# Kernel optimization log

Hardware: AMD Instinct MI355X
Metric: run time of the kernel (lower is better)

Reference implementation:

```python
import jax, jax.numpy as jnp
import numpy as np

STD = 0.02

def setup_inputs() -> dict:
    key = jax.random.key(0)
    k1, k2, k3 = jax.random.split(key, 3)
    b, n_t, n, n_h = 2, 2048, 256, 8
    r_prime = jax.random.normal(k1, (b, n_t, n), dtype=jnp.float32)
    Q = STD * jax.random.normal(k2, (n_h, n, n), dtype=jnp.float32)
    E = STD * jax.random.normal(k3, (n_h, n, n), dtype=jnp.float32)
    return {"r_prime": r_prime, "Q": Q, "E": E}

def reference(r_prime, Q, E):
    # Omega[b,h,t,u] = sum_ij r'[b,t,i] Q[h,i,j] r'[b,u,j]
    Omega = jnp.einsum('bti,hij,buj->bhtu', r_prime, Q, r_prime)
    n_t = r_prime.shape[1]
    mask = jnp.tril(jnp.ones((n_t, n_t), dtype=r_prime.dtype))  # causal
    Omega = Omega * mask  # broadcast over (b, h)
    # r[b,t,i] = sum_{h,u,j} Omega[b,h,t,u] E[h,i,j] r'[b,u,j]
    r = jnp.einsum('bhtu,hij,buj->bti', Omega, E, r_prime)
    return r
```

## Files before the change

### kernel.cpp

```cpp
#include <hip/hip_runtime.h>
#include <hip/hip_bf16.h>

typedef __bf16 bf16x8 __attribute__((ext_vector_type(8)));
typedef float f32x4 __attribute__((ext_vector_type(4)));
typedef float f32x16 __attribute__((ext_vector_type(16)));

#define NB 2
#define NT 2048
#define ND 256
#define NH 8

__device__ inline __bf16 to_bf16(float f) {
  union { __hip_bfloat16 h; __bf16 b; } u;
  u.h = __float2bfloat16(f);
  return u.b;
}
__device__ inline float bf2f(__bf16 b) {
  union { __bf16 b; unsigned short s; } u; u.b = b;
  union { unsigned int i; float f; } v; v.i = ((unsigned int)u.s) << 16;
  return v.f;
}

typedef __attribute__((address_space(1))) const void g1void;
typedef __attribute__((address_space(3))) void l3void;

__device__ inline void gl_lds16(const void* g, void* l) {
  __builtin_amdgcn_global_load_lds((g1void*)g, (l3void*)l, 16, 0, 0);
}

__device__ inline void stage_tile64_t256(const __bf16* gsrc, __bf16* lds, int tid) {
  const char* wub = (const char*)lds + (tid & ~63) * 16;
#pragma unroll
  for (int p = 0; p < 8; ++p) {
    int lin = p * 256 + tid;
    int row = lin >> 5, c = lin & 31;
    const __bf16* g = gsrc + row * 256 + ((c ^ (row & 31)) << 3);
    gl_lds16((const void*)g, (void*)(wub + p * 4096));
  }
}

__device__ inline void stage_R64(const __bf16* gsrc, __bf16* lds, int w, int lane) {
#pragma unroll
  for (int p = 0; p < 4; ++p) {
    int lin = (p * 8 + w) * 64 + lane;
    int row = lin >> 5, c = lin & 31;
    const __bf16* g = gsrc + row * 256 + ((c ^ (row & 31)) << 3);
    gl_lds16((const void*)g, (void*)((char*)lds + (size_t)(p * 8 + w) * 1024));
  }
}
__device__ inline void stage_V64(const __bf16* gsrc, __bf16* lds, int w, int lane) {
#pragma unroll
  for (int p = 0; p < 4; ++p) {
    int lin = (p * 8 + w) * 64 + lane;
    int row = lin >> 3, c = lin & 7;
    const __bf16* g = gsrc + (size_t)row * NT + ((c ^ (row & 7)) << 3);
    gl_lds16((const void*)g, (void*)((char*)lds + (size_t)(p * 8 + w) * 1024));
  }
}

__global__ __launch_bounds__(256) void prep_kernel(
    const float* __restrict__ r, const float* __restrict__ Q,
    const float* __restrict__ E, __bf16* __restrict__ Rb,
    __bf16* __restrict__ Qt, __bf16* __restrict__ Eb) {
  __shared__ float T[32][33];
  int bx = blockIdx.x;
  if (bx < 512) {
    int h = bx >> 6, i0 = ((bx >> 3) & 7) * 32, j0 = (bx & 7) * 32;
    int rr = threadIdx.x >> 3, c4 = (threadIdx.x & 7) * 4;
    f32x4 v = *(const f32x4*)(Q + h * 65536 + (i0 + rr) * 256 + j0 + c4);
#pragma unroll
    for (int j = 0; j < 4; ++j) T[rr][c4 + j] = v[j];
    __syncthreads();
    __bf16* dst = Qt + h * 65536 + (j0 + rr) * 256 + i0 + c4;
#pragma unroll
    for (int j = 0; j < 4; ++j) dst[j] = to_bf16(T[c4 + j][rr]);
  } else {
    int idx = (bx - 512) * 256 + threadIdx.x;
    const int nR = NB * NT * ND;
    const int nQ = NH * ND * ND;
    const int stride = 1024 * 256;
    for (; idx < nR + nQ; idx += stride) {
      if (idx < nR) Rb[idx] = to_bf16(r[idx]);
      else Eb[idx - nR] = to_bf16(E[idx - nR]);
    }
  }
}

__global__ __launch_bounds__(256, 4) void gemm_stage1(
    const __bf16* __restrict__ Rb, const __bf16* __restrict__ Qt,
    const __bf16* __restrict__ Eb, __bf16* __restrict__ Am,
    __bf16* __restrict__ Vt) {
  __shared__ __bf16 Bs[64 * 256];
  int z = blockIdx.z, x = blockIdx.x;
  const __bf16 *A, *B;
  __bf16* C;
  int m0, n0, cstride;
  if (z < 16) {
    int bb = z >> 3, h = z & 7;
    A = Rb + (size_t)bb * NT * ND;
    B = Qt + (size_t)h * ND * ND;
    C = Am + (size_t)z * NT * ND;
    m0 = (x & 31) * 64; n0 = (x >> 5) * 64; cstride = ND;
  } else {
    int zz = z - 16;
    int bb = zz >> 3, h = zz & 7;
    A = Eb + (size_t)h * ND * ND;
    B = Rb + (size_t)bb * NT * ND;
    C = Vt + (size_t)zz * ND * NT;
    m0 = (x & 3) * 64; n0 = (x >> 2) * 64; cstride = NT;
  }

  int tid = threadIdx.x;
  int lane = tid & 63, w = tid >> 6;
  int l15 = lane & 15, lg = lane >> 4;

  stage_tile64_t256(B + (size_t)n0 * 256, Bs, tid);

  bf16x8 af[8];
  const __bf16* arow = A + (size_t)(m0 + w * 16 + l15) * 256 + lg * 8;
#pragma unroll
  for (int ks = 0; ks < 8; ++ks) af[ks] = *(const bf16x8*)(arow + ks * 32);

  __syncthreads();

  f32x4 acc[4] = {};
#pragma unroll
  for (int ks = 0; ks < 8; ++ks) {
#pragma unroll
    for (int nt = 0; nt < 4; ++nt) {
      int row = nt * 16 + l15;
      int ch = (ks * 4 + lg) ^ (row & 31);
      bf16x8 bfr = *(const bf16x8*)(&Bs[row * 256 + ch * 8]);
      acc[nt] = __builtin_amdgcn_mfma_f32_16x16x32_bf16(af[ks], bfr, acc[nt], 0, 0, 0);
    }
  }
#pragma unroll
  for (int nt = 0; nt < 4; ++nt)
#pragma unroll
    for (int m = 0; m < 4; ++m)
      C[(size_t)(m0 + w * 16 + lg * 4 + m) * cstride + n0 + nt * 16 + l15] =
          to_bf16(acc[nt][m]);
}

__global__ __launch_bounds__(512, 2) void attn_kernel(
    const __bf16* __restrict__ Am, const __bf16* __restrict__ Rb,
    const __bf16* __restrict__ Vt, __bf16* __restrict__ partial,
    float* __restrict__ out, int use_partial) {
  __shared__ __bf16 Rk[2][64 * 256];
  __shared__ __bf16 Vk[2][256 * 64];
  __shared__ __bf16 Sl[128 * 64];

  int xx = blockIdx.x & 7, kk = blockIdx.x >> 3;
  int z = xx + 8 * (kk & 1);
  int local = kk >> 1;
  int px = local >> 1, q = local & 1;
  int b = z >> 3, h = z & 7;

  const __bf16* Amat = Am + (size_t)z * NT * ND;
  const __bf16* R = Rb + (size_t)b * NT * ND;
  const __bf16* V = Vt + (size_t)z * ND * NT;

  int tid = threadIdx.x;
  int w = tid >> 6, lane = tid & 63;
  int l31 = lane & 31, l5 = lane >> 5;
  int swt = w >> 1, swu = w & 1;

#pragma unroll 1
  for (int half = 0; half < 2; ++half) {
    int tt = half ? (15 - px) : px;
    int t0 = tt * 128;
    int ulast = 2 * tt + 1;

    bf16x8 af[16];
    {
      const __bf16* arow = Amat + (size_t)(t0 + swt * 32 + l31) * ND + l5 * 8;
#pragma unroll
      for (int ks = 0; ks < 16; ++ks) af[ks] = *(const bf16x8*)(arow + ks * 16);
    }
    stage_R64(R + (size_t)q * 64 * 256, &Rk[0][0], w, lane);
    stage_V64(V + q * 64, &Vk[0][0], w, lane);

    f32x16 acc[4] = {};

    asm volatile("s_waitcnt vmcnt(4)" ::: "memory");
    __builtin_amdgcn_s_barrier();

    int buf = 0;
#pragma unroll 1
    for (int ut = q; ut <= ulast; ut += 2) {
      int u0 = ut * 64;
      bool has_next = (ut + 2 <= ulast);
      if (has_next) {
        stage_R64(R + (size_t)(ut + 2) * 64 * 256, &Rk[buf ^ 1][0], w, lane);
        stage_V64(V + (ut + 2) * 64, &Vk[buf ^ 1][0], w, lane);
      }

      const __bf16* Rcur = &Rk[buf][0];
      int bbase = (swu * 32 + l31) * 256;
      f32x16 s0 = {}, s1 = {};
#pragma unroll
      for (int ks = 0; ks < 8; ++ks) {
        bf16x8 bfr = *(const bf16x8*)(Rcur + bbase + (((ks * 2 + l5) ^ l31) << 3));
        s0 = __builtin_amdgcn_mfma_f32_32x32x16_bf16(af[ks], bfr, s0, 0, 0, 0);
      }
#pragma unroll
      for (int ks = 8; ks < 16; ++ks) {
        bf16x8 bfr = *(const bf16x8*)(Rcur + bbase + (((ks * 2 + l5) ^ l31) << 3));
        s1 = __builtin_amdgcn_mfma_f32_32x32x16_bf16(af[ks], bfr, s1, 0, 0, 0);
      }
      f32x16 s = s0 + s1;

      int ucol = u0 + swu * 32 + l31;
      int cg = swu * 4 + (l31 >> 3);
#pragma unroll
      for (int rg = 0; rg < 16; ++rg) {
        int trow = (rg & 3) + 8 * (rg >> 2) + 4 * l5;
        int srow = swt * 32 + trow;
        float v = (ucol <= t0 + srow) ? s[rg] : 0.0f;
        Sl[srow * 64 + ((cg ^ (srow & 7)) << 3) + (l31 & 7)] = to_bf16(v);
      }
      asm volatile("s_waitcnt lgkmcnt(0)" ::: "memory");
      if (has_next) asm volatile("s_waitcnt vmcnt(8)" ::: "memory");
      else          asm volatile("s_waitcnt vmcnt(0)" ::: "memory");
      __builtin_amdgcn_s_barrier();

      bf16x8 sf[4];
      int srow2 = swt * 32 + l31;
#pragma unroll
      for (int ks = 0; ks < 4; ++ks) {
        int c = (ks * 2 + l5) ^ (srow2 & 7);
        sf[ks] = *(const bf16x8*)(Sl + srow2 * 64 + c * 8);
      }
      const __bf16* Vcur = &Vk[buf][0];
#pragma unroll
      for (int it = 0; it < 4; ++it) {
        int irow = swu * 128 + it * 32 + l31;
#pragma unroll
        for (int ks = 0; ks < 4; ++ks) {
          int c = (ks * 2 + l5) ^ (irow & 7);
          bf16x8 vf = *(const bf16x8*)(Vcur + irow * 64 + c * 8);
          acc[it] = __builtin_amdgcn_mfma_f32_32x32x16_bf16(sf[ks], vf, acc[it], 0, 0, 0);
        }
      }
      if (has_next) asm volatile("s_waitcnt vmcnt(4)" ::: "memory");
      else          asm volatile("s_waitcnt vmcnt(0)" ::: "memory");
      __builtin_amdgcn_s_barrier();
      buf ^= 1;
    }

    __syncthreads();
    __bf16* Ep = &Rk[0][0];
#pragma unroll
    for (int it = 0; it < 4; ++it)
#pragma unroll
      for (int rg = 0; rg < 16; ++rg) {
        int trow = (rg & 3) + 8 * (rg >> 2) + 4 * l5;
        Ep[(swt * 32 + trow) * 256 + swu * 128 + it * 32 + l31] = to_bf16(acc[it][rg]);
      }
    __syncthreads();
    if (use_partial) {
      __bf16* Pdst = partial + ((size_t)(q * NH + h) * NB + b) * NT * ND +
                     (size_t)t0 * ND;
#pragma unroll
      for (int c = 0; c < 8; ++c) {
        int off = c * 512 + tid;
        *(bf16x8*)(Pdst + off * 8) = *(const bf16x8*)(Ep + off * 8);
      }
    } else {
      float* O = out + (size_t)b * NT * ND + (size_t)t0 * ND;
#pragma unroll
      for (int c = 0; c < 8; ++c) {
        int off = c * 512 + tid;
        bf16x8 vv = *(const bf16x8*)(Ep + off * 8);
#pragma unroll
        for (int e = 0; e < 8; ++e) atomicAdd(&O[off * 8 + e], bf2f(vv[e]));
      }
    }
    __syncthreads();
  }
}

__global__ __launch_bounds__(256) void reduce_kernel(
    const __bf16* __restrict__ partial, float* __restrict__ out) {
  size_t gid = (size_t)blockIdx.x * 256 + threadIdx.x;
  size_t e = gid * 8;
  int bb = (int)(e >> 19);
  size_t x = e & ((1u << 19) - 1);
  float sum[8] = {};
#pragma unroll
  for (int s = 0; s < 16; ++s) {
    bf16x8 v = *(const bf16x8*)(partial + (((size_t)(s * NB + bb)) << 19) + x);
#pragma unroll
    for (int j = 0; j < 8; ++j) sum[j] += bf2f(v[j]);
  }
  f32x4 lo = {sum[0], sum[1], sum[2], sum[3]};
  f32x4 hi = {sum[4], sum[5], sum[6], sum[7]};
  *(f32x4*)(out + e) = lo;
  *(f32x4*)(out + e + 4) = hi;
}

extern "C" void kernel_launch(void* const* d_in, const int* in_sizes, int n_in,
                              void* d_out, int out_size, void* d_ws, size_t ws_size,
                              hipStream_t stream) {
  const float* r = (const float*)d_in[0];
  const float* Q = (const float*)d_in[1];
  const float* E = (const float*)d_in[2];
  float* out = (float*)d_out;

  char* ws = (char*)d_ws;
  __bf16* Rb = (__bf16*)(ws);
  __bf16* Qt = (__bf16*)(ws + (2u << 20));
  __bf16* Eb = (__bf16*)(ws + (3u << 20));
  __bf16* Am = (__bf16*)(ws + (4u << 20));
  __bf16* Vt = (__bf16*)(ws + (20u << 20));
  __bf16* Pq = (__bf16*)(ws + (36u << 20));
  int use_partial = (ws_size >= (72ull << 20)) ? 1 : 0;

  if (!use_partial)
    hipMemsetAsync(d_out, 0, (size_t)out_size * sizeof(float), stream);

  prep_kernel<<<1536, 256, 0, stream>>>(r, Q, E, Rb, Qt, Eb);

  gemm_stage1<<<dim3(128, 1, 32), 256, 0, stream>>>(Rb, Qt, Eb, Am, Vt);

  attn_kernel<<<dim3(256), 512, 0, stream>>>(Am, Rb, Vt, Pq, out, use_partial);

  if (use_partial) reduce_kernel<<<512, 256, 0, stream>>>(Pq, out);
}
```

Baseline: 150.7 us.

## Drop LDS double buffering and split attention into 512 blocks for higher occupancy

The attention kernel no longer loops over two time tiles per block. It launches 512 blocks, one tile each, and sends heavy tiles first. The LDS double buffer for R and V becomes a single buffer, which halves shared memory so launch bounds can ask for 4 blocks per CU. This trades explicit prefetch overlap for overlap between co-resident blocks, and every iteration now waits for a full load with vmcnt(0).

```diff
diff --git a/kernel.cpp b/kernel.cpp
--- a/kernel.cpp
+++ b/kernel.cpp
@@ -142,18 +142,23 @@
           to_bf16(acc[nt][m]);
 }
 
-__global__ __launch_bounds__(512, 2) void attn_kernel(
+__global__ __launch_bounds__(512, 4) void attn_kernel(
     const __bf16* __restrict__ Am, const __bf16* __restrict__ Rb,
     const __bf16* __restrict__ Vt, __bf16* __restrict__ partial,
     float* __restrict__ out, int use_partial) {
-  __shared__ __bf16 Rk[2][64 * 256];
-  __shared__ __bf16 Vk[2][256 * 64];
-  __shared__ __bf16 Sl[128 * 64];
-
-  int xx = blockIdx.x & 7, kk = blockIdx.x >> 3;
-  int z = xx + 8 * (kk & 1);
-  int local = kk >> 1;
-  int px = local >> 1, q = local & 1;
+  __shared__ __bf16 LDSA[(64 * 256) + (256 * 64) + (128 * 64)];
+  __bf16* Rk = LDSA;
+  __bf16* Vk = LDSA + 64 * 256;
+  __bf16* Sl = LDSA + 64 * 256 * 2;
+
+  int half = blockIdx.x >> 8;
+  int idx = blockIdx.x & 255;
+  int xcd = idx & 7;
+  int j = idx >> 3;
+  int z = xcd + 8 * (j & 1);
+  int q = (j >> 1) & 1;
+  int t3 = j >> 2;
+  int tt = half ? t3 : 15 - t3;
   int b = z >> 3, h = z & 7;
 
   const __bf16* Amat = Am + (size_t)z * NT * ND;
@@ -165,118 +170,99 @@
   int l31 = lane & 31, l5 = lane >> 5;
   int swt = w >> 1, swu = w & 1;
 
+  int t0 = tt * 128;
+  int ulast = 2 * tt + 1;
+
+  bf16x8 af[16];
+  {
+    const __bf16* arow = Amat + (size_t)(t0 + swt * 32 + l31) * ND + l5 * 8;
+#pragma unroll
+    for (int ks = 0; ks < 16; ++ks) af[ks] = *(const bf16x8*)(arow + ks * 16);
+  }
+
+  f32x16 acc[4] = {};
+
 #pragma unroll 1
-  for (int half = 0; half < 2; ++half) {
-    int tt = half ? (15 - px) : px;
-    int t0 = tt * 128;
-    int ulast = 2 * tt + 1;
-
-    bf16x8 af[16];
-    {
-      const __bf16* arow = Amat + (size_t)(t0 + swt * 32 + l31) * ND + l5 * 8;
-#pragma unroll
-      for (int ks = 0; ks < 16; ++ks) af[ks] = *(const bf16x8*)(arow + ks * 16);
-    }
-    stage_R64(R + (size_t)q * 64 * 256, &Rk[0][0], w, lane);
-    stage_V64(V + q * 64, &Vk[0][0], w, lane);
-
-    f32x16 acc[4] = {};
-
-    asm volatile("s_waitcnt vmcnt(4)" ::: "memory");
+  for (int ut = q; ut <= ulast; ut += 2) {
+    int u0 = ut * 64;
+    stage_R64(R + (size_t)u0 * 256, Rk, w, lane);
+    stage_V64(V + u0, Vk, w, lane);
+    asm volatile("s_waitcnt vmcnt(0)" ::: "memory");
     __builtin_amdgcn_s_barrier();
 
-    int buf = 0;
-#pragma unroll 1
-    for (int ut = q; ut <= ulast; ut += 2) {
-      int u0 = ut * 64;
-      bool has_next = (ut + 2 <= ulast);
-      if (has_next) {
-        stage_R64(R + (size_t)(ut + 2) * 64 * 256, &Rk[buf ^ 1][0], w, lane);
-        stage_V64(V + (ut + 2) * 64, &Vk[buf ^ 1][0], w, lane);
+    int bbase = (swu * 32 + l31) * 256;
+    f32x16 s0 = {}, s1 = {};
+#pragma unroll
+    for (int ks = 0; ks < 8; ++ks) {
+      bf16x8 bfr = *(const bf16x8*)(Rk + bbase + (((ks * 2 + l5) ^ l31) << 3));
+      s0 = __builtin_amdgcn_mfma_f32_32x32x16_bf16(af[ks], bfr, s0, 0, 0, 0);
+    }
+#pragma unroll
+    for (int ks = 8; ks < 16; ++ks) {
+      bf16x8 bfr = *(const bf16x8*)(Rk + bbase + (((ks * 2 + l5) ^ l31) << 3));
+      s1 = __builtin_amdgcn_mfma_f32_32x32x16_bf16(af[ks], bfr, s1, 0, 0, 0);
+    }
+    f32x16 s = s0 + s1;
+
+    int ucol = u0 + swu * 32 + l31;
+    int cg = swu * 4 + (l31 >> 3);
+#pragma unroll
+    for (int rg = 0; rg < 16; ++rg) {
+      int trow = (rg & 3) + 8 * (rg >> 2) + 4 * l5;
+      int srow = swt * 32 + trow;
+      float v = (ucol <= t0 + srow) ? s[rg] : 0.0f;
+      Sl[srow * 64 + ((cg ^ (srow & 7)) << 3) + (l31 & 7)] = to_bf16(v);
+    }
+    asm volatile("s_waitcnt lgkmcnt(0)" ::: "memory");
+    __builtin_amdgcn_s_barrier();
+
+    bf16x8 sf[4];
+    int srow2 = swt * 32 + l31;
+#pragma unroll
+    for (int ks = 0; ks < 4; ++ks) {
+      int c = (ks * 2 + l5) ^ (srow2 & 7);
+      sf[ks] = *(const bf16x8*)(Sl + srow2 * 64 + c * 8);
+    }
+#pragma unroll
+    for (int it = 0; it < 4; ++it) {
+      int irow = swu * 128 + it * 32 + l31;
+#pragma unroll
+      for (int ks = 0; ks < 4; ++ks) {
+        int c = (ks * 2 + l5) ^ (irow & 7);
+        bf16x8 vf = *(const bf16x8*)(Vk + irow * 64 + c * 8);
+        acc[it] = __builtin_amdgcn_mfma_f32_32x32x16_bf16(sf[ks], vf, acc[it], 0, 0, 0);
       }
-
-      const __bf16* Rcur = &Rk[buf][0];
-      int bbase = (swu * 32 + l31) * 256;
-      f32x16 s0 = {}, s1 = {};
-#pragma unroll
-      for (int ks = 0; ks < 8; ++ks) {
-        bf16x8 bfr = *(const bf16x8*)(Rcur + bbase + (((ks * 2 + l5) ^ l31) << 3));
-        s0 = __builtin_amdgcn_mfma_f32_32x32x16_bf16(af[ks], bfr, s0, 0, 0, 0);
-      }
-#pragma unroll
-      for (int ks = 8; ks < 16; ++ks) {
-        bf16x8 bfr = *(const bf16x8*)(Rcur + bbase + (((ks * 2 + l5) ^ l31) << 3));
-        s1 = __builtin_amdgcn_mfma_f32_32x32x16_bf16(af[ks], bfr, s1, 0, 0, 0);
-      }
-      f32x16 s = s0 + s1;
-
-      int ucol = u0 + swu * 32 + l31;
-      int cg = swu * 4 + (l31 >> 3);
-#pragma unroll
-      for (int rg = 0; rg < 16; ++rg) {
-        int trow = (rg & 3) + 8 * (rg >> 2) + 4 * l5;
-        int srow = swt * 32 + trow;
-        float v = (ucol <= t0 + srow) ? s[rg] : 0.0f;
-        Sl[srow * 64 + ((cg ^ (srow & 7)) << 3) + (l31 & 7)] = to_bf16(v);
-      }
-      asm volatile("s_waitcnt lgkmcnt(0)" ::: "memory");
-      if (has_next) asm volatile("s_waitcnt vmcnt(8)" ::: "memory");
-      else          asm volatile("s_waitcnt vmcnt(0)" ::: "memory");
-      __builtin_amdgcn_s_barrier();
-
-      bf16x8 sf[4];
-      int srow2 = swt * 32 + l31;
-#pragma unroll
-      for (int ks = 0; ks < 4; ++ks) {
-        int c = (ks * 2 + l5) ^ (srow2 & 7);
-        sf[ks] = *(const bf16x8*)(Sl + srow2 * 64 + c * 8);
-      }
-      const __bf16* Vcur = &Vk[buf][0];
-#pragma unroll
-      for (int it = 0; it < 4; ++it) {
-        int irow = swu * 128 + it * 32 + l31;
-#pragma unroll
-        for (int ks = 0; ks < 4; ++ks) {
-          int c = (ks * 2 + l5) ^ (irow & 7);
-          bf16x8 vf = *(const bf16x8*)(Vcur + irow * 64 + c * 8);
-          acc[it] = __builtin_amdgcn_mfma_f32_32x32x16_bf16(sf[ks], vf, acc[it], 0, 0, 0);
-        }
-      }
-      if (has_next) asm volatile("s_waitcnt vmcnt(4)" ::: "memory");
-      else          asm volatile("s_waitcnt vmcnt(0)" ::: "memory");
-      __builtin_amdgcn_s_barrier();
-      buf ^= 1;
-    }
-
-    __syncthreads();
-    __bf16* Ep = &Rk[0][0];
-#pragma unroll
-    for (int it = 0; it < 4; ++it)
-#pragma unroll
-      for (int rg = 0; rg < 16; ++rg) {
-        int trow = (rg & 3) + 8 * (rg >> 2) + 4 * l5;
-        Ep[(swt * 32 + trow) * 256 + swu * 128 + it * 32 + l31] = to_bf16(acc[it][rg]);
-      }
-    __syncthreads();
-    if (use_partial) {
-      __bf16* Pdst = partial + ((size_t)(q * NH + h) * NB + b) * NT * ND +
-                     (size_t)t0 * ND;
-#pragma unroll
-      for (int c = 0; c < 8; ++c) {
-        int off = c * 512 + tid;
-        *(bf16x8*)(Pdst + off * 8) = *(const bf16x8*)(Ep + off * 8);
-      }
-    } else {
-      float* O = out + (size_t)b * NT * ND + (size_t)t0 * ND;
-#pragma unroll
-      for (int c = 0; c < 8; ++c) {
-        int off = c * 512 + tid;
-        bf16x8 vv = *(const bf16x8*)(Ep + off * 8);
-#pragma unroll
-        for (int e = 0; e < 8; ++e) atomicAdd(&O[off * 8 + e], bf2f(vv[e]));
-      }
-    }
-    __syncthreads();
+    }
+    __builtin_amdgcn_s_barrier();
+  }
+
+  __syncthreads();
+  __bf16* Ep = LDSA;
+#pragma unroll
+  for (int it = 0; it < 4; ++it)
+#pragma unroll
+    for (int rg = 0; rg < 16; ++rg) {
+      int trow = (rg & 3) + 8 * (rg >> 2) + 4 * l5;
+      Ep[(swt * 32 + trow) * 256 + swu * 128 + it * 32 + l31] = to_bf16(acc[it][rg]);
+    }
+  __syncthreads();
+  if (use_partial) {
+    __bf16* Pdst = partial + ((size_t)(q * NH + h) * NB + b) * NT * ND +
+                   (size_t)t0 * ND;
+#pragma unroll
+    for (int c = 0; c < 8; ++c) {
+      int off = c * 512 + tid;
+      *(bf16x8*)(Pdst + off * 8) = *(const bf16x8*)(Ep + off * 8);
+    }
+  } else {
+    float* O = out + (size_t)b * NT * ND + (size_t)t0 * ND;
+#pragma unroll
+    for (int c = 0; c < 8; ++c) {
+      int off = c * 512 + tid;
+      bf16x8 vv = *(const bf16x8*)(Ep + off * 8);
+#pragma unroll
+      for (int e = 0; e < 8; ++e) atomicAdd(&O[off * 8 + e], bf2f(vv[e]));
+    }
   }
 }
 
@@ -323,7 +309,7 @@
 
   gemm_stage1<<<dim3(128, 1, 32), 256, 0, stream>>>(Rb, Qt, Eb, Am, Vt);
 
-  attn_kernel<<<dim3(256), 512, 0, stream>>>(Am, Rb, Vt, Pq, out, use_partial);
+  attn_kernel<<<dim3(512), 512, 0, stream>>>(Am, Rb, Vt, Pq, out, use_partial);
 
   if (use_partial) reduce_kernel<<<512, 256, 0, stream>>>(Pq, out);
 }
```

After: 354.8 us. +135.4%, slower.
